# Kernel optimization log

Hardware: AMD Instinct MI355X
Metric: run time of the kernel (lower is better)

Reference implementation:

```python
import jax, jax.numpy as jnp
import numpy as np

EMBED_DIM = 1024
WINDOW = 256
NUM_HEADS = 16
HEAD_DIM = EMBED_DIM // NUM_HEADS
SCALE = HEAD_DIM ** (-0.5)


def setup_inputs() -> dict:
    key = jax.random.key(0)
    ks = jax.random.split(key, 9)
    B, S, E = 4, 4096, EMBED_DIM
    std = E ** (-0.5)
    x = jax.random.normal(ks[0], (B, S, E), dtype=jnp.float32)
    Wq = jax.random.normal(ks[1], (E, E), dtype=jnp.float32) * std
    Wk = jax.random.normal(ks[2], (E, E), dtype=jnp.float32) * std
    Wv = jax.random.normal(ks[3], (E, E), dtype=jnp.float32) * std
    Wo = jax.random.normal(ks[4], (E, E), dtype=jnp.float32) * std
    bq = jax.random.normal(ks[5], (E,), dtype=jnp.float32) * 0.01
    bk = jax.random.normal(ks[6], (E,), dtype=jnp.float32) * 0.01
    bv = jax.random.normal(ks[7], (E,), dtype=jnp.float32) * 0.01
    bo = jax.random.normal(ks[8], (E,), dtype=jnp.float32) * 0.01
    return {"x": x, "Wq": Wq, "bq": bq, "Wk": Wk, "bk": bk,
            "Wv": Wv, "bv": bv, "Wo": Wo, "bo": bo}


def reference(x, Wq, bq, Wk, bk, Wv, bv, Wo, bo):
    B, S, E = x.shape
    W = WINDOW
    nw = S // W  # seq_len chosen divisible by window_size
    # projections (torch Linear: x @ W.T + b); no head split in the original
    q = x @ Wq.T + bq
    k = x @ Wk.T + bk
    v = x @ Wv.T + bv
    # split into non-overlapping windows: [B, nw, W, E]
    qw = q.reshape(B, nw, W, E)
    kw = k.reshape(B, nw, W, E)
    vw = v.reshape(B, nw, W, E)
    scores = jnp.einsum('bnqe,bnke->bnqk', qw, kw) * SCALE  # [B, nw, W, W]
    causal = jnp.tril(jnp.ones((W, W), dtype=bool))
    scores = jnp.where(causal, scores, -jnp.inf)
    attn = jax.nn.softmax(scores, axis=-1)
    out = jnp.einsum('bnqk,bnke->bnqe', attn, vw).reshape(B, S, E)
    out = out @ Wo.T + bo
    return out + x
```

## Files before the change

### kernel.cpp

```cpp
#include <hip/hip_runtime.h>
#include <hip/hip_bf16.h>


typedef unsigned short u16;
typedef __attribute__((ext_vector_type(8))) short short8;
typedef __attribute__((ext_vector_type(4))) short short4v;
typedef __attribute__((ext_vector_type(4))) float f32x4;

__device__ __forceinline__ u16 f2bf(float f) {
    __hip_bfloat16 h = __float2bfloat16(f);
    return __builtin_bit_cast(u16, h);
}

__global__ void cast_f32_bf16(const float* __restrict__ src, u16* __restrict__ dst, int n) {
    int i = (blockIdx.x * 256 + threadIdx.x) * 8;
    if (i >= n) return;
    const float4* s = (const float4*)(src + i);
    float4 a = s[0], b = s[1];
    short8 o;
    o[0] = (short)f2bf(a.x); o[1] = (short)f2bf(a.y); o[2] = (short)f2bf(a.z); o[3] = (short)f2bf(a.w);
    o[4] = (short)f2bf(b.x); o[5] = (short)f2bf(b.y); o[6] = (short)f2bf(b.z); o[7] = (short)f2bf(b.w);
    *(short8*)(dst + i) = o;
}

__global__ void wcast(const float* __restrict__ Wq, const float* __restrict__ Wk,
                      const float* __restrict__ Wv, const float* __restrict__ Wo,
                      u16* __restrict__ WqT, u16* __restrict__ WkT,
                      u16* __restrict__ WvT, u16* __restrict__ Wob)
{
    __shared__ float lt[64][65];
    const int which = blockIdx.x >> 8;
    const int bid = blockIdx.x & 255;
    const int c0 = (bid & 15) * 64, r0 = (bid >> 4) * 64;
    const int t = threadIdx.x;
    const int tr = t >> 3, tc = (t & 7) * 8;
    const float* src = which == 0 ? Wq : which == 1 ? Wk : which == 2 ? Wv : Wo;
    if (which == 3) {
#pragma unroll
        for (int p = 0; p < 2; ++p) {
            int r = p * 32 + tr;
            const float* s = src + (size_t)(r0 + r) * 1024 + c0 + tc;
            float4 a = *(const float4*)s, b = *(const float4*)(s + 4);
            short8 o;
            o[0] = (short)f2bf(a.x); o[1] = (short)f2bf(a.y); o[2] = (short)f2bf(a.z); o[3] = (short)f2bf(a.w);
            o[4] = (short)f2bf(b.x); o[5] = (short)f2bf(b.y); o[6] = (short)f2bf(b.z); o[7] = (short)f2bf(b.w);
            *(short8*)(Wob + (size_t)(r0 + r) * 1024 + c0 + tc) = o;
        }
        return;
    }
    u16* dst = which == 0 ? WqT : which == 1 ? WkT : WvT;
#pragma unroll
    for (int p = 0; p < 2; ++p) {
        int r = p * 32 + tr;
        const float* s = src + (size_t)(r0 + r) * 1024 + c0 + tc;
        float4 a = *(const float4*)s, b = *(const float4*)(s + 4);
        lt[r][tc + 0] = a.x; lt[r][tc + 1] = a.y; lt[r][tc + 2] = a.z; lt[r][tc + 3] = a.w;
        lt[r][tc + 4] = b.x; lt[r][tc + 5] = b.y; lt[r][tc + 6] = b.z; lt[r][tc + 7] = b.w;
    }
    __syncthreads();
#pragma unroll
    for (int p = 0; p < 2; ++p) {
        int r = p * 32 + tr;
        short8 o;
#pragma unroll
        for (int j = 0; j < 8; ++j) o[j] = (short)f2bf(lt[tc + j][r]);
        *(short8*)(dst + (size_t)(c0 + r) * 1024 + r0 + tc) = o;
    }
}

__global__ void ub2(const float* __restrict__ Wk, const float* __restrict__ bq,
                    const float* __restrict__ Wo, const float* __restrict__ bv,
                    const float* __restrict__ bo, float* __restrict__ u, float* __restrict__ b2)
{
    const int t = threadIdx.x, bid = blockIdx.x;
    if (bid < 4) {
        int b = bid * 256 + t;
        float acc = 0.f;
        for (int o = 0; o < 1024; ++o) acc += Wk[(size_t)o * 1024 + b] * bq[o];
        u[b] = acc;
    } else {
        int n = (bid - 4) * 16 + (t >> 4);
        int l = t & 15;
        float acc = 0.f;
        for (int m = l; m < 1024; m += 16) acc += Wo[(size_t)n * 1024 + m] * bv[m];
#pragma unroll
        for (int s = 1; s < 16; s <<= 1) acc += __shfl_xor(acc, s, 64);
        if (l == 0) b2[n] = acc + bo[n];
    }
}

__global__ __launch_bounds__(256, 4) void gemm_small_dual(
    const u16* __restrict__ HA, const u16* __restrict__ HB, u16* __restrict__ HC,
    const u16* __restrict__ WA, const u16* __restrict__ WB, u16* __restrict__ WC)
{
    __shared__ __align__(16) u16 At[64 * 64], Bt[64 * 64];
    const bool sec = blockIdx.x >= 256;
    const u16* A = sec ? WA : HA;
    const u16* B = sec ? WB : HB;
    u16* C = sec ? WC : HC;
    const int bid = blockIdx.x & 255;
    const int m0 = (bid >> 4) * 64, n0 = (bid & 15) * 64;
    const int t = threadIdx.x, lane = t & 63, w = t >> 6;
    const int l15 = lane & 15, lk = lane >> 4;

    f32x4 acc[4];
#pragma unroll
    for (int m = 0; m < 4; ++m) acc[m] = (f32x4){0.f, 0.f, 0.f, 0.f};

    for (int k0 = 0; k0 < 1024; k0 += 64) {
        __syncthreads();
#pragma unroll
        for (int p = 0; p < 2; ++p) {
            int e = p * 2048 + t * 8;
            int row = e >> 6, col = e & 63;
            short8 va = *(const short8*)(A + (size_t)(m0 + row) * 1024 + k0 + col);
            *(short8*)((char*)At + row * 128 + ((col * 2) ^ ((row & 7) << 4))) = va;
            short8 vb = *(const short8*)(B + (size_t)(n0 + row) * 1024 + k0 + col);
            *(short8*)((char*)Bt + row * 128 + ((col * 2) ^ ((row & 7) << 4))) = vb;
        }
        __syncthreads();
#pragma unroll
        for (int ks = 0; ks < 2; ++ks) {
            int bc = ks * 64 + lk * 16;
            int brow = w * 16 + l15;
            short8 bfr = *(const short8*)((char*)Bt + brow * 128 + (bc ^ ((brow & 7) << 4)));
#pragma unroll
            for (int m = 0; m < 4; ++m) {
                int arow = m * 16 + l15;
                short8 af = *(const short8*)((char*)At + arow * 128 + (bc ^ ((arow & 7) << 4)));
                acc[m] = __builtin_amdgcn_mfma_f32_16x16x32_bf16(af, bfr, acc[m], 0, 0, 0);
            }
        }
    }
#pragma unroll
    for (int m = 0; m < 4; ++m)
#pragma unroll
        for (int r = 0; r < 4; ++r) {
            int row = m0 + m * 16 + lk * 4 + r;
            int col = n0 + w * 16 + l15;
            C[(size_t)row * 1024 + col] = f2bf(acc[m][r]);
        }
}

__global__ __launch_bounds__(256, 2) void gemm_yv(
    const u16* __restrict__ A, const u16* __restrict__ BH, const u16* __restrict__ BW,
    const float* __restrict__ ub, u16* __restrict__ Y, u16* __restrict__ V2t)
{
    __shared__ __align__(16) u16 At[128 * 64];
    __shared__ __align__(16) u16 Bt[128 * 64];
    const int t = threadIdx.x;
    const int lane = t & 63;
    const int wid = t >> 6;
    const int wm = wid >> 1, wn = wid & 1;
    const int l15 = lane & 15, lk = lane >> 4;
    const int K = 1024;

    const int bid = blockIdx.y * gridDim.x + blockIdx.x;
    const int cpx = 2048 >> 3;
    const int swz = (bid & 7) * cpx + (bid >> 3);
    const int tn = swz & 15;
    const int tm = swz >> 4;
    const int m0 = tm * 128;
    const bool isv = tn >= 8;
    const int n0 = (tn & 7) * 128;
    const u16* B = isv ? BW : BH;

    f32x4 acc[4][4];
#pragma unroll
    for (int m = 0; m < 4; ++m)
#pragma unroll
        for (int n = 0; n < 4; ++n)
            acc[m][n] = (f32x4){0.f, 0.f, 0.f, 0.f};

    for (int k0 = 0; k0 < K; k0 += 64) {
        __syncthreads();
#pragma unroll
        for (int p = 0; p < 4; ++p) {
            int e = p * 2048 + t * 8;
            int row = e >> 6, col = e & 63;
            short8 va = *(const short8*)(A + (size_t)(m0 + row) * K + k0 + col);
            *(short8*)((char*)At + row * 128 + ((col * 2) ^ ((row & 7) << 4))) = va;
            short8 vb = *(const short8*)(B + (size_t)(n0 + row) * K + k0 + col);
            *(short8*)((char*)Bt + row * 128 + ((col * 2) ^ ((row & 7) << 4))) = vb;
        }
        __syncthreads();
#pragma unroll
        for (int ks = 0; ks < 2; ++ks) {
            const int bc = ks * 64 + lk * 16;
            short8 af[4], bfr[4];
#pragma unroll
            for (int m = 0; m < 4; ++m) {
                int row = wm * 64 + m * 16 + l15;
                af[m] = *(const short8*)((char*)At + row * 128 + (bc ^ ((row & 7) << 4)));
            }
#pragma unroll
            for (int n = 0; n < 4; ++n) {
                int row = wn * 64 + n * 16 + l15;
                bfr[n] = *(const short8*)((char*)Bt + row * 128 + (bc ^ ((row & 7) << 4)));
            }
#pragma unroll
            for (int m = 0; m < 4; ++m)
#pragma unroll
                for (int n = 0; n < 4; ++n)
                    acc[m][n] = __builtin_amdgcn_mfma_f32_16x16x32_bf16(af[m], bfr[n], acc[m][n], 0, 0, 0);
        }
    }

    if (!isv) {
#pragma unroll
        for (int m = 0; m < 4; ++m)
#pragma unroll
            for (int n = 0; n < 4; ++n) {
                int col = n0 + wn * 64 + n * 16 + l15;
                float bv = ub[col];
#pragma unroll
                for (int r = 0; r < 4; ++r) {
                    int row = m0 + wm * 64 + m * 16 + lk * 4 + r;
                    Y[(size_t)row * 1024 + col] = f2bf(acc[m][n][r] + bv);
                }
            }
    } else {
#pragma unroll
        for (int m = 0; m < 4; ++m)
#pragma unroll
            for (int n = 0; n < 4; ++n) {
                int col = n0 + wn * 64 + n * 16 + l15;
                int row0 = m0 + wm * 64 + m * 16 + lk * 4;
                short4v pk;
#pragma unroll
                for (int r = 0; r < 4; ++r) pk[r] = (short)f2bf(acc[m][n][r]);
                *(short4v*)(V2t + (size_t)col * 16384 + row0) = pk;
            }
    }
}

__global__ __launch_bounds__(256, 2) void attn_win(
    const u16* __restrict__ y, const u16* __restrict__ xb,
    const u16* __restrict__ vt, const float* __restrict__ xres,
    const float* __restrict__ b2, float* __restrict__ outp)
{
    __shared__ __align__(16) char smem[54272];
    u16* Qt = (u16*)smem;
    u16* Kt = (u16*)(smem + 4096);
    u16* Vl = (u16*)smem;
    u16* P  = (u16*)(smem + 36864);
    float* rmax = (float*)(smem + 53248);
    float* rsum = (float*)(smem + 53760);

    const int t = threadIdx.x;
    const int lane = t & 63, wv = t >> 6;
    const int l15 = lane & 15, lk = lane >> 4;
    const int bid = blockIdx.x;
    const int swz = (bid & 7) * 64 + (bid >> 3);
    const int win = swz >> 3, qc = swz & 7;
    const size_t qrow0 = (size_t)win * 256 + qc * 32;
    const size_t krow0 = (size_t)win * 256;

    f32x4 acc[2][4];
#pragma unroll
    for (int m = 0; m < 2; ++m)
#pragma unroll
        for (int n = 0; n < 4; ++n)
            acc[m][n] = (f32x4){0.f, 0.f, 0.f, 0.f};

    for (int e0 = 0; e0 < 1024; e0 += 64) {
        __syncthreads();
        {
            int row = t >> 3, col = (t & 7) * 8;
            short8 v = *(const short8*)(y + (qrow0 + row) * 1024 + e0 + col);
            *(short8*)((char*)Qt + row * 128 + ((col * 2) ^ ((row & 7) << 4))) = v;
        }
#pragma unroll
        for (int p = 0; p < 8; ++p) {
            int e = p * 2048 + t * 8;
            int row = e >> 6, col = e & 63;
            short8 v = *(const short8*)(xb + (krow0 + row) * 1024 + e0 + col);
            *(short8*)((char*)Kt + row * 128 + ((col * 2) ^ ((row & 7) << 4))) = v;
        }
        __syncthreads();
#pragma unroll
        for (int ks = 0; ks < 2; ++ks) {
            const int bc = ks * 64 + lk * 16;
            short8 af[2], bfr[4];
#pragma unroll
            for (int m = 0; m < 2; ++m) {
                int row = m * 16 + l15;
                af[m] = *(const short8*)((char*)Qt + row * 128 + (bc ^ ((row & 7) << 4)));
            }
#pragma unroll
            for (int n = 0; n < 4; ++n) {
                int row = wv * 64 + n * 16 + l15;
                bfr[n] = *(const short8*)((char*)Kt + row * 128 + (bc ^ ((row & 7) << 4)));
            }
            __builtin_amdgcn_s_setprio(1);
#pragma unroll
            for (int m = 0; m < 2; ++m)
#pragma unroll
                for (int n = 0; n < 4; ++n)
                    acc[m][n] = __builtin_amdgcn_mfma_f32_16x16x32_bf16(af[m], bfr[n], acc[m][n], 0, 0, 0);
            __builtin_amdgcn_s_setprio(0);
        }
    }

#pragma unroll
    for (int m = 0; m < 2; ++m)
#pragma unroll
        for (int n = 0; n < 4; ++n) {
            int col = wv * 64 + n * 16 + l15;
#pragma unroll
            for (int r = 0; r < 4; ++r) {
                int qpos = qc * 32 + m * 16 + lk * 4 + r;
                float v = acc[m][n][r] * 0.125f;
                acc[m][n][r] = (col <= qpos) ? v : -1e30f;
            }
        }
#pragma unroll
    for (int m = 0; m < 2; ++m)
#pragma unroll
        for (int r = 0; r < 4; ++r) {
            float tmx = fmaxf(fmaxf(acc[m][0][r], acc[m][1][r]), fmaxf(acc[m][2][r], acc[m][3][r]));
            tmx = fmaxf(tmx, __shfl_xor(tmx, 1));
            tmx = fmaxf(tmx, __shfl_xor(tmx, 2));
            tmx = fmaxf(tmx, __shfl_xor(tmx, 4));
            tmx = fmaxf(tmx, __shfl_xor(tmx, 8));
            if (l15 == 0) rmax[(m * 16 + lk * 4 + r) * 4 + wv] = tmx;
        }
    __syncthreads();
#pragma unroll
    for (int m = 0; m < 2; ++m)
#pragma unroll
        for (int r = 0; r < 4; ++r) {
            int row = m * 16 + lk * 4 + r;
            float m4 = fmaxf(fmaxf(rmax[row * 4], rmax[row * 4 + 1]),
                             fmaxf(rmax[row * 4 + 2], rmax[row * 4 + 3]));
            float s = 0.f;
#pragma unroll
            for (int n = 0; n < 4; ++n) {
                float e = __expf(acc[m][n][r] - m4);
                acc[m][n][r] = e;
                s += e;
            }
            s += __shfl_xor(s, 1);
            s += __shfl_xor(s, 2);
            s += __shfl_xor(s, 4);
            s += __shfl_xor(s, 8);
            if (l15 == 0) rsum[row * 4 + wv] = s;
        }
    __syncthreads();
#pragma unroll
    for (int m = 0; m < 2; ++m)
#pragma unroll
        for (int r = 0; r < 4; ++r) {
            int row = m * 16 + lk * 4 + r;
            float inv = 1.f / (rsum[row * 4] + rsum[row * 4 + 1] + rsum[row * 4 + 2] + rsum[row * 4 + 3]);
#pragma unroll
            for (int n = 0; n < 4; ++n) {
                int col = wv * 64 + n * 16 + l15;
                *(u16*)((char*)P + row * 512 + ((col * 2) ^ ((row & 7) << 4))) = f2bf(acc[m][n][r] * inv);
            }
        }

    for (int n0 = 0; n0 < 1024; n0 += 64) {
        __syncthreads();
#pragma unroll
        for (int p = 0; p < 8; ++p) {
            int e = p * 2048 + t * 8;
            int row = e >> 8, col = e & 255;
            short8 v = *(const short8*)(vt + (size_t)(n0 + row) * 16384 + win * 256 + col);
            *(short8*)((char*)Vl + row * 512 + ((col * 2) ^ ((row & 7) << 4))) = v;
        }
        __syncthreads();
        f32x4 acc2[2];
#pragma unroll
        for (int m = 0; m < 2; ++m) acc2[m] = (f32x4){0.f, 0.f, 0.f, 0.f};
#pragma unroll
        for (int ks = 0; ks < 8; ++ks) {
            const int bc = ks * 64 + lk * 16;
            short8 af[2];
#pragma unroll
            for (int m = 0; m < 2; ++m) {
                int row = m * 16 + l15;
                af[m] = *(const short8*)((char*)P + row * 512 + (bc ^ ((row & 7) << 4)));
            }
            int vrow = wv * 16 + l15;
            short8 bfr = *(const short8*)((char*)Vl + vrow * 512 + (bc ^ ((vrow & 7) << 4)));
            __builtin_amdgcn_s_setprio(1);
#pragma unroll
            for (int m = 0; m < 2; ++m)
                acc2[m] = __builtin_amdgcn_mfma_f32_16x16x32_bf16(af[m], bfr, acc2[m], 0, 0, 0);
            __builtin_amdgcn_s_setprio(0);
        }
#pragma unroll
        for (int m = 0; m < 2; ++m) {
#pragma unroll
            for (int r = 0; r < 4; ++r) {
                int row = m * 16 + lk * 4 + r;
                int col = n0 + wv * 16 + l15;
                size_t idx = (qrow0 + row) * 1024 + col;
                outp[idx] = acc2[m][r] + b2[col] + xres[idx];
            }
        }
    }
}

extern "C" void kernel_launch(void* const* d_in, const int* in_sizes, int n_in,
                              void* d_out, int out_size, void* d_ws, size_t ws_size,
                              hipStream_t stream) {
    const float* x  = (const float*)d_in[0];
    const float* Wq = (const float*)d_in[1];
    const float* bq = (const float*)d_in[2];
    const float* Wk = (const float*)d_in[3];
    const float* Wv = (const float*)d_in[5];
    const float* bv = (const float*)d_in[6];
    const float* Wo = (const float*)d_in[7];
    const float* bo = (const float*)d_in[8];
    float* out = (float*)d_out;

    char* ws = (char*)d_ws;
    u16* xb  = (u16*)(ws);
    u16* yb  = (u16*)(ws + 33554432);
    u16* v2t = (u16*)(ws + 67108864);
    u16* WqT = (u16*)(ws + 100663296);
    u16* WkT = (u16*)(ws + 102760448);
    u16* WvT = (u16*)(ws + 104857600);
    u16* Wob = (u16*)(ws + 106954752);
    u16* Hb  = (u16*)(ws + 109051904);
    u16* W2b = (u16*)(ws + 111149056);
    float* u_  = (float*)(ws + 113246208);
    float* b2_ = (float*)(ws + 113250304);

    cast_f32_bf16<<<8192, 256, 0, stream>>>(x, xb, 16777216);
    wcast<<<1024, 256, 0, stream>>>(Wq, Wk, Wv, Wo, WqT, WkT, WvT, Wob);
    ub2<<<68, 256, 0, stream>>>(Wk, bq, Wo, bv, bo, u_, b2_);
    gemm_small_dual<<<512, 256, 0, stream>>>(WkT, WqT, Hb, Wob, WvT, W2b);
    gemm_yv<<<dim3(16, 128), 256, 0, stream>>>(xb, Hb, W2b, u_, yb, v2t);
    attn_win<<<512, 256, 0, stream>>>(yb, xb, v2t, x, b2_, out);
}
```

Measured before the change: 212.6 us.

## Use direct global-to-LDS loads in gemm_yv and drop LDS staging in attention

The projection GEMM now stages A and B tiles with global_load_lds (direct global-to-LDS DMA) and a lane-XOR swizzle, so tile data no longer passes through registers. The attention kernel drops LDS staging of Q/K and V and reads MFMA operands straight from global memory, which relies on L2/cache reuse. It also preloads the whole P tile into registers once, which cuts shared memory to about 17KB and raises the occupancy hint to 4 blocks. The risks are uncoalesced, repeated global reads in attention and higher register pressure from pa[8][2].

```diff
diff --git a/kernel.cpp b/kernel.cpp
--- a/kernel.cpp
+++ b/kernel.cpp
@@ -10,6 +10,13 @@
 __device__ __forceinline__ u16 f2bf(float f) {
     __hip_bfloat16 h = __float2bfloat16(f);
     return __builtin_bit_cast(u16, h);
+}
+
+__device__ __forceinline__ void gl_lds16(const u16* g, u16* l) {
+    __builtin_amdgcn_global_load_lds(
+        (const __attribute__((address_space(1))) void*)g,
+        (__attribute__((address_space(3))) void*)l,
+        16, 0, 0);
 }
 
 __global__ void cast_f32_bf16(const float* __restrict__ src, u16* __restrict__ dst, int n) {
@@ -146,12 +153,12 @@
     const u16* __restrict__ A, const u16* __restrict__ BH, const u16* __restrict__ BW,
     const float* __restrict__ ub, u16* __restrict__ Y, u16* __restrict__ V2t)
 {
-    __shared__ __align__(16) u16 At[128 * 64];
-    __shared__ __align__(16) u16 Bt[128 * 64];
+    __shared__ __align__(16) u16 At[8192];
+    __shared__ __align__(16) u16 Bt[8192];
     const int t = threadIdx.x;
     const int lane = t & 63;
-    const int wid = t >> 6;
-    const int wm = wid >> 1, wn = wid & 1;
+    const int w = t >> 6;
+    const int wm = w >> 1, wn = w & 1;
     const int l15 = lane & 15, lk = lane >> 4;
     const int K = 1024;
 
@@ -165,6 +172,9 @@
     const int n0 = (tn & 7) * 128;
     const u16* B = isv ? BW : BH;
 
+    const int sr = lane >> 3;
+    const int ss = (lane & 7) ^ sr;
+
     f32x4 acc[4][4];
 #pragma unroll
     for (int m = 0; m < 4; ++m)
@@ -175,13 +185,10 @@
     for (int k0 = 0; k0 < K; k0 += 64) {
         __syncthreads();
 #pragma unroll
-        for (int p = 0; p < 4; ++p) {
-            int e = p * 2048 + t * 8;
-            int row = e >> 6, col = e & 63;
-            short8 va = *(const short8*)(A + (size_t)(m0 + row) * K + k0 + col);
-            *(short8*)((char*)At + row * 128 + ((col * 2) ^ ((row & 7) << 4))) = va;
-            short8 vb = *(const short8*)(B + (size_t)(n0 + row) * K + k0 + col);
-            *(short8*)((char*)Bt + row * 128 + ((col * 2) ^ ((row & 7) << 4))) = vb;
+        for (int c = 0; c < 4; ++c) {
+            int row = c * 32 + w * 8 + sr;
+            gl_lds16(A + (size_t)(m0 + row) * K + k0 + ss * 8, At + c * 2048 + w * 512);
+            gl_lds16(B + (size_t)(n0 + row) * K + k0 + ss * 8, Bt + c * 2048 + w * 512);
         }
         __syncthreads();
 #pragma unroll
@@ -234,18 +241,15 @@
     }
 }
 
-__global__ __launch_bounds__(256, 2) void attn_win(
+__global__ __launch_bounds__(256, 4) void attn_win(
     const u16* __restrict__ y, const u16* __restrict__ xb,
     const u16* __restrict__ vt, const float* __restrict__ xres,
     const float* __restrict__ b2, float* __restrict__ outp)
 {
-    __shared__ __align__(16) char smem[54272];
-    u16* Qt = (u16*)smem;
-    u16* Kt = (u16*)(smem + 4096);
-    u16* Vl = (u16*)smem;
-    u16* P  = (u16*)(smem + 36864);
-    float* rmax = (float*)(smem + 53248);
-    float* rsum = (float*)(smem + 53760);
+    __shared__ __align__(16) char smem[17408];
+    u16* P  = (u16*)smem;
+    float* rmax = (float*)(smem + 16384);
+    float* rsum = (float*)(smem + 16896);
 
     const int t = threadIdx.x;
     const int lane = t & 63, wv = t >> 6;
@@ -264,34 +268,16 @@
             acc[m][n] = (f32x4){0.f, 0.f, 0.f, 0.f};
 
     for (int e0 = 0; e0 < 1024; e0 += 64) {
-        __syncthreads();
-        {
-            int row = t >> 3, col = (t & 7) * 8;
-            short8 v = *(const short8*)(y + (qrow0 + row) * 1024 + e0 + col);
-            *(short8*)((char*)Qt + row * 128 + ((col * 2) ^ ((row & 7) << 4))) = v;
-        }
-#pragma unroll
-        for (int p = 0; p < 8; ++p) {
-            int e = p * 2048 + t * 8;
-            int row = e >> 6, col = e & 63;
-            short8 v = *(const short8*)(xb + (krow0 + row) * 1024 + e0 + col);
-            *(short8*)((char*)Kt + row * 128 + ((col * 2) ^ ((row & 7) << 4))) = v;
-        }
-        __syncthreads();
 #pragma unroll
         for (int ks = 0; ks < 2; ++ks) {
-            const int bc = ks * 64 + lk * 16;
+            const int co = e0 + ks * 32 + lk * 8;
             short8 af[2], bfr[4];
 #pragma unroll
-            for (int m = 0; m < 2; ++m) {
-                int row = m * 16 + l15;
-                af[m] = *(const short8*)((char*)Qt + row * 128 + (bc ^ ((row & 7) << 4)));
-            }
-#pragma unroll
-            for (int n = 0; n < 4; ++n) {
-                int row = wv * 64 + n * 16 + l15;
-                bfr[n] = *(const short8*)((char*)Kt + row * 128 + (bc ^ ((row & 7) << 4)));
-            }
+            for (int m = 0; m < 2; ++m)
+                af[m] = *(const short8*)(y + (qrow0 + m * 16 + l15) * 1024 + co);
+#pragma unroll
+            for (int n = 0; n < 4; ++n)
+                bfr[n] = *(const short8*)(xb + (krow0 + wv * 64 + n * 16 + l15) * 1024 + co);
             __builtin_amdgcn_s_setprio(1);
 #pragma unroll
             for (int m = 0; m < 2; ++m)
@@ -359,35 +345,29 @@
                 *(u16*)((char*)P + row * 512 + ((col * 2) ^ ((row & 7) << 4))) = f2bf(acc[m][n][r] * inv);
             }
         }
+    __syncthreads();
+
+    short8 pa[8][2];
+#pragma unroll
+    for (int ks = 0; ks < 8; ++ks)
+#pragma unroll
+        for (int m = 0; m < 2; ++m) {
+            int row = m * 16 + l15;
+            pa[ks][m] = *(const short8*)((char*)P + row * 512 + ((ks * 64 + lk * 16) ^ ((row & 7) << 4)));
+        }
 
     for (int n0 = 0; n0 < 1024; n0 += 64) {
-        __syncthreads();
-#pragma unroll
-        for (int p = 0; p < 8; ++p) {
-            int e = p * 2048 + t * 8;
-            int row = e >> 8, col = e & 255;
-            short8 v = *(const short8*)(vt + (size_t)(n0 + row) * 16384 + win * 256 + col);
-            *(short8*)((char*)Vl + row * 512 + ((col * 2) ^ ((row & 7) << 4))) = v;
-        }
-        __syncthreads();
         f32x4 acc2[2];
 #pragma unroll
         for (int m = 0; m < 2; ++m) acc2[m] = (f32x4){0.f, 0.f, 0.f, 0.f};
 #pragma unroll
         for (int ks = 0; ks < 8; ++ks) {
-            const int bc = ks * 64 + lk * 16;
-            short8 af[2];
-#pragma unroll
-            for (int m = 0; m < 2; ++m) {
-                int row = m * 16 + l15;
-                af[m] = *(const short8*)((char*)P + row * 512 + (bc ^ ((row & 7) << 4)));
-            }
-            int vrow = wv * 16 + l15;
-            short8 bfr = *(const short8*)((char*)Vl + vrow * 512 + (bc ^ ((vrow & 7) << 4)));
+            short8 bfr = *(const short8*)(vt + (size_t)(n0 + wv * 16 + l15) * 16384
+                                             + win * 256 + ks * 32 + lk * 8);
             __builtin_amdgcn_s_setprio(1);
 #pragma unroll
             for (int m = 0; m < 2; ++m)
-                acc2[m] = __builtin_amdgcn_mfma_f32_16x16x32_bf16(af[m], bfr, acc2[m], 0, 0, 0);
+                acc2[m] = __builtin_amdgcn_mfma_f32_16x16x32_bf16(pa[ks][m], bfr, acc2[m], 0, 0, 0);
             __builtin_amdgcn_s_setprio(0);
         }
 #pragma unroll
```

Measured after the change: 236.6 us. 1.11x slower.
